# Kernel optimization log

Hardware: AMD Instinct MI355X
Metric: run time of the kernel (lower is better)

## Reference

```python
import jax, jax.numpy as jnp
import numpy as np

BS, DEG, H = 32, 4, 32
OUT = H  # n_aggr=1 inside Full -> out_size = n_aggr * h_size = h_size


def setup_inputs() -> dict:
    key = jax.random.key(0)
    k1, k2 = jax.random.split(key)
    neighbour_h = jax.random.normal(k1, (BS, DEG, H), dtype=jnp.float32)
    hp1 = H + 1
    t_shape = (hp1,) * DEG + (OUT,)  # [33,33,33,33,32]
    # xavier_uniform-like scale: fan_in = hp1**DEG, fan_out = OUT
    scale = float(np.sqrt(2.0 / (hp1 ** DEG + OUT)))
    T = jax.random.normal(k2, t_shape, dtype=jnp.float32) * scale
    return {"neighbour_h": neighbour_h, "T": T}


def reference(neighbour_h, T):
    # Full.forward: chunk neighbour_h along child dim, feed to AugmentedTensor.
    # AugmentedTensor: sequentially contract T against each child's augmented
    # embedding [h_i ; 1] over the leading axes of T.
    bs, deg, h = neighbour_h.shape
    hp1 = h + 1
    # augment with trailing 1 (bias slot): [bs, deg, h+1]
    h_aug = jnp.concatenate(
        [neighbour_h, jnp.ones((bs, deg, 1), neighbour_h.dtype)], axis=2
    )
    # first contraction: [bs, hp1] @ [hp1, hp1^(deg-1)*out]
    res = jnp.matmul(h_aug[:, 0, :], T.reshape(hp1, -1))
    # remaining contractions shrink the trailing dim by hp1 each step
    for i in range(1, deg):
        res = jnp.einsum("bi,bio->bo", h_aug[:, i, :], res.reshape(bs, hp1, -1))
    return res  # [bs, out_size] == [bs, h_size] since n_aggr=1
```

## Files before the change

kernel.cpp:

```cpp
#include <hip/hip_runtime.h>
#include <hip/hip_bf16.h>

#define HSZ 32
#define HP1 33
#define M3 35937
#define M3P 35952
#define TI_STRIDE 1149984
#define NBLK 2247
#define NT 64

#define OFF_A0T   0
#define OFF_D     8192
#define OFF_TILES 4610048

typedef short bf16x8 __attribute__((ext_vector_type(8)));
typedef float f32x16 __attribute__((ext_vector_type(16)));

__device__ inline short f2bf(float f) {
  __hip_bfloat16 h = __float2bfloat16(f);
  return __builtin_bit_cast(short, h);
}

__global__ __launch_bounds__(256) void k_pre(const float* __restrict__ nh,
                                             float* __restrict__ a0T,
                                             float* __restrict__ D,
                                             float* __restrict__ tiles) {
  const int b = blockIdx.y;
  const int m = blockIdx.x * 256 + threadIdx.x;
  if (m < M3P) {
    float v = 0.f;
    if (m < M3) {
      const int j = m / 1089;
      const int r = m - j * 1089;
      const int k = r / 33;
      const int l = r - k * 33;
      const float a1 = (j < HSZ) ? nh[(b * 4 + 1) * HSZ + j] : 1.0f;
      const float a2 = (k < HSZ) ? nh[(b * 4 + 2) * HSZ + k] : 1.0f;
      const float a3 = (l < HSZ) ? nh[(b * 4 + 3) * HSZ + l] : 1.0f;
      v = a1 * a2 * a3;
    }
    D[(size_t)b * M3P + m] = v;
  }
  if (blockIdx.x == 0 && threadIdx.x < HP1) {
    const int i = threadIdx.x;
    a0T[i * 32 + b] = (i < HSZ) ? nh[(b * 4 + 0) * HSZ + i] : 1.0f;
  }
  if (b == 1 && blockIdx.x < 64) {
    ((float4*)tiles)[blockIdx.x * 256 + threadIdx.x] =
        make_float4(0.f, 0.f, 0.f, 0.f);
  }
}

__global__ __launch_bounds__(64) void k_main(const float* __restrict__ T,
                                             const float* __restrict__ a0T,
                                             const float* __restrict__ D,
                                             float* __restrict__ tiles) {
  const int blk = blockIdx.x;
  const int m0 = blk * 16;
  const int l = (int)threadIdx.x;
  const int bo = l & 31;
  const int g = l >> 5;

  const float* dp = D + (size_t)bo * M3P + m0 + 8 * g;
  float df[8];
  *(float4*)(df)     = *(const float4*)(dp);
  *(float4*)(df + 4) = *(const float4*)(dp + 4);

  size_t toff[8];
#pragma unroll
  for (int e = 0; e < 8; ++e) {
    int mm = m0 + 8 * g + e;
    if (mm > M3 - 1) mm = M3 - 1;
    toff[e] = (size_t)mm * 32 + bo;
  }

  f32x16 acc = {};

  float tv[8];
#pragma unroll
  for (int e = 0; e < 8; ++e) tv[e] = T[toff[e]];
  float a0c = a0T[bo];

  for (int i = 0; i < HP1; ++i) {
    float tn[8];
    float a0n = 0.f;
    if (i < HP1 - 1) {
      const float* Tn = T + (size_t)(i + 1) * TI_STRIDE;
#pragma unroll
      for (int e = 0; e < 8; ++e) tn[e] = Tn[toff[e]];
      a0n = a0T[(i + 1) * 32 + bo];
    }
    bf16x8 af, bfr;
#pragma unroll
    for (int e = 0; e < 8; ++e) {
      af[e]  = f2bf(a0c * df[e]);
      bfr[e] = f2bf(tv[e]);
    }
    acc = __builtin_amdgcn_mfma_f32_32x32x16_bf16(af, bfr, acc, 0, 0, 0);
#pragma unroll
    for (int e = 0; e < 8; ++e) tv[e] = tn[e];
    a0c = a0n;
  }

  float* tp = tiles + (size_t)(blk & (NT - 1)) * 1024;
#pragma unroll
  for (int r = 0; r < 16; ++r) {
    const int brow = (r & 3) + 8 * (r >> 2) + 4 * g;
    atomicAdd(tp + brow * 32 + bo, acc[r]);
  }
}

__global__ __launch_bounds__(256) void k_red(const float* __restrict__ tiles,
                                             float* __restrict__ out) {
  const int idx = blockIdx.x * 256 + (int)threadIdx.x;
  float s = 0.f;
  for (int t = 0; t < NT; ++t) s += tiles[(size_t)t * 1024 + idx];
  out[idx] = s;
}

extern "C" void kernel_launch(void* const* d_in, const int* in_sizes, int n_in,
                              void* d_out, int out_size, void* d_ws, size_t ws_size,
                              hipStream_t stream) {
  const float* nh = (const float*)d_in[0];
  const float* T  = (const float*)d_in[1];
  float* out = (float*)d_out;
  char* ws = (char*)d_ws;
  float* a0T   = (float*)(ws + OFF_A0T);
  float* D     = (float*)(ws + OFF_D);
  float* tiles = (float*)(ws + OFF_TILES);

  k_pre<<<dim3(141, 32), 256, 0, stream>>>(nh, a0T, D, tiles);
  k_main<<<NBLK, 64, 0, stream>>>(T, a0T, D, tiles);
  k_red<<<4, 256, 0, stream>>>(tiles, out);
}
```

Baseline: 42.63 us.

## Stream T rows into LDS with async global_load_lds eight-deep pipeline

Result: faster. 40.18 us (-5.8%).

```diff
diff --git a/kernel.cpp b/kernel.cpp
--- a/kernel.cpp
+++ b/kernel.cpp
@@ -6,8 +6,10 @@
 #define M3 35937
 #define M3P 35952
 #define TI_STRIDE 1149984
+#define TIB ((size_t)TI_STRIDE * 4)
 #define NBLK 2247
 #define NT 64
+#define DEPTH 8
 
 #define OFF_A0T   0
 #define OFF_D     8192
@@ -55,6 +57,7 @@
                                              const float* __restrict__ a0T,
                                              const float* __restrict__ D,
                                              float* __restrict__ tiles) {
+  __shared__ float lds[DEPTH * 512];
   const int blk = blockIdx.x;
   const int m0 = blk * 16;
   const int l = (int)threadIdx.x;
@@ -66,41 +69,74 @@
   *(float4*)(df)     = *(const float4*)(dp);
   *(float4*)(df + 4) = *(const float4*)(dp + 4);
 
-  size_t toff[8];
+  float a0v[HP1];
 #pragma unroll
-  for (int e = 0; e < 8; ++e) {
-    int mm = m0 + 8 * g + e;
-    if (mm > M3 - 1) mm = M3 - 1;
-    toff[e] = (size_t)mm * 32 + bo;
+  for (int i = 0; i < HP1; ++i) a0v[i] = a0T[i * 32 + bo];
+
+  {
+    float dsum = 0.f, asum = 0.f;
+#pragma unroll
+    for (int e = 0; e < 8; ++e) dsum += df[e];
+#pragma unroll
+    for (int i = 0; i < HP1; ++i) asum += a0v[i];
+    asm volatile("" :: "v"(dsum), "v"(asum) : "memory");
   }
+
+  const int mrel = l >> 3;
+  const size_t src0 = (m0 + mrel < M3) ? ((size_t)(m0 * 32 + l * 4) * 4) : 0;
+  const size_t src1 =
+      (m0 + 8 + mrel < M3) ? ((size_t)(m0 * 32 + 256 + l * 4) * 4) : 0;
+  const char* Tb = (const char*)T;
+
+#define ISSUE(row_, slot_)                                                   \
+  {                                                                          \
+    const char* s0p_ = Tb + (size_t)(row_)*TIB + src0;                       \
+    const char* s1p_ = Tb + (size_t)(row_)*TIB + src1;                       \
+    __builtin_amdgcn_global_load_lds(                                        \
+        (const __attribute__((address_space(1))) void*)s0p_,                 \
+        (__attribute__((address_space(3))) void*)(&lds[(slot_)*512]),        \
+        16, 0, 0);                                                           \
+    __builtin_amdgcn_global_load_lds(                                        \
+        (const __attribute__((address_space(1))) void*)s1p_,                 \
+        (__attribute__((address_space(3))) void*)(&lds[(slot_)*512 + 256]),  \
+        16, 0, 0);                                                           \
+  }
+
+  ISSUE(0, 0) ISSUE(1, 1) ISSUE(2, 2) ISSUE(3, 3)
+  ISSUE(4, 4) ISSUE(5, 5) ISSUE(6, 6) ISSUE(7, 7)
 
   f32x16 acc = {};
 
-  float tv[8];
-#pragma unroll
-  for (int e = 0; e < 8; ++e) tv[e] = T[toff[e]];
-  float a0c = a0T[bo];
+#define STEP(i_, vm_, doIssue_)                                              \
+  {                                                                          \
+    asm volatile("s_waitcnt vmcnt(" #vm_ ")" ::: "memory");                  \
+    __builtin_amdgcn_sched_barrier(0);                                       \
+    float tvv[8];                                                            \
+    _Pragma("unroll")                                                        \
+    for (int e = 0; e < 8; ++e)                                              \
+      tvv[e] = lds[((i_) % DEPTH) * 512 + (8 * g + e) * 32 + bo];            \
+    asm volatile("s_waitcnt lgkmcnt(0)" ::: "memory");                       \
+    if (doIssue_) ISSUE((i_) + DEPTH, (i_) % DEPTH)                          \
+    bf16x8 af, bfr;                                                          \
+    _Pragma("unroll")                                                        \
+    for (int e = 0; e < 8; ++e) {                                            \
+      af[e] = f2bf(a0v[i_] * df[e]);                                         \
+      bfr[e] = f2bf(tvv[e]);                                                 \
+    }                                                                        \
+    acc = __builtin_amdgcn_mfma_f32_32x32x16_bf16(af, bfr, acc, 0, 0, 0);    \
+  }
 
-  for (int i = 0; i < HP1; ++i) {
-    float tn[8];
-    float a0n = 0.f;
-    if (i < HP1 - 1) {
-      const float* Tn = T + (size_t)(i + 1) * TI_STRIDE;
-#pragma unroll
-      for (int e = 0; e < 8; ++e) tn[e] = Tn[toff[e]];
-      a0n = a0T[(i + 1) * 32 + bo];
-    }
-    bf16x8 af, bfr;
-#pragma unroll
-    for (int e = 0; e < 8; ++e) {
-      af[e]  = f2bf(a0c * df[e]);
-      bfr[e] = f2bf(tv[e]);
-    }
-    acc = __builtin_amdgcn_mfma_f32_32x32x16_bf16(af, bfr, acc, 0, 0, 0);
-#pragma unroll
-    for (int e = 0; e < 8; ++e) tv[e] = tn[e];
-    a0c = a0n;
-  }
+  STEP(0, 14, 1)  STEP(1, 14, 1)  STEP(2, 14, 1)  STEP(3, 14, 1)
+  STEP(4, 14, 1)  STEP(5, 14, 1)  STEP(6, 14, 1)  STEP(7, 14, 1)
+  STEP(8, 14, 1)  STEP(9, 14, 1)  STEP(10, 14, 1) STEP(11, 14, 1)
+  STEP(12, 14, 1) STEP(13, 14, 1) STEP(14, 14, 1) STEP(15, 14, 1)
+  STEP(16, 14, 1) STEP(17, 14, 1) STEP(18, 14, 1) STEP(19, 14, 1)
+  STEP(20, 14, 1) STEP(21, 14, 1) STEP(22, 14, 1) STEP(23, 14, 1)
+  STEP(24, 14, 1) STEP(25, 14, 0) STEP(26, 12, 0) STEP(27, 10, 0)
+  STEP(28, 8, 0)  STEP(29, 6, 0)  STEP(30, 4, 0)  STEP(31, 2, 0)
+  STEP(32, 0, 0)
+#undef STEP
+#undef ISSUE
 
   float* tp = tiles + (size_t)(blk & (NT - 1)) * 1024;
 #pragma unroll
```

## Stream T through LDS with async global_load_lds multi-stage pipeline, double work per block

Applied to the files above, without the earlier changes.

After: 39.75 us. 1.07x faster.

```diff
diff --git a/kernel.cpp b/kernel.cpp
--- a/kernel.cpp
+++ b/kernel.cpp
@@ -4,14 +4,16 @@
 #define HSZ 32
 #define HP1 33
 #define M3 35937
-#define M3P 35952
+#define M3P2 35968
 #define TI_STRIDE 1149984
-#define NBLK 2247
+#define TIB ((size_t)TI_STRIDE * 4)
+#define NBLK 1124
 #define NT 64
+#define DEPTH 6
 
 #define OFF_A0T   0
 #define OFF_D     8192
-#define OFF_TILES 4610048
+#define OFF_TILES 4612096
 
 typedef short bf16x8 __attribute__((ext_vector_type(8)));
 typedef float f32x16 __attribute__((ext_vector_type(16)));
@@ -27,7 +29,7 @@
                                              float* __restrict__ tiles) {
   const int b = blockIdx.y;
   const int m = blockIdx.x * 256 + threadIdx.x;
-  if (m < M3P) {
+  if (m < M3P2) {
     float v = 0.f;
     if (m < M3) {
       const int j = m / 1089;
@@ -39,7 +41,7 @@
       const float a3 = (l < HSZ) ? nh[(b * 4 + 3) * HSZ + l] : 1.0f;
       v = a1 * a2 * a3;
     }
-    D[(size_t)b * M3P + m] = v;
+    D[(size_t)b * M3P2 + m] = v;
   }
   if (blockIdx.x == 0 && threadIdx.x < HP1) {
     const int i = threadIdx.x;
@@ -55,52 +57,94 @@
                                              const float* __restrict__ a0T,
                                              const float* __restrict__ D,
                                              float* __restrict__ tiles) {
+  __shared__ float lds[DEPTH * 1024];
   const int blk = blockIdx.x;
-  const int m0 = blk * 16;
+  const int m0 = blk * 32;
   const int l = (int)threadIdx.x;
   const int bo = l & 31;
   const int g = l >> 5;
 
-  const float* dp = D + (size_t)bo * M3P + m0 + 8 * g;
-  float df[8];
-  *(float4*)(df)     = *(const float4*)(dp);
-  *(float4*)(df + 4) = *(const float4*)(dp + 4);
+  const float* dp = D + (size_t)bo * M3P2 + m0 + 8 * g;
+  float df0[8], df1[8];
+  *(float4*)(df0)     = *(const float4*)(dp);
+  *(float4*)(df0 + 4) = *(const float4*)(dp + 4);
+  *(float4*)(df1)     = *(const float4*)(dp + 16);
+  *(float4*)(df1 + 4) = *(const float4*)(dp + 20);
 
-  size_t toff[8];
+  float a0v[HP1];
 #pragma unroll
-  for (int e = 0; e < 8; ++e) {
-    int mm = m0 + 8 * g + e;
-    if (mm > M3 - 1) mm = M3 - 1;
-    toff[e] = (size_t)mm * 32 + bo;
+  for (int i = 0; i < HP1; ++i) a0v[i] = a0T[i * 32 + bo];
+
+  {
+    float s = 0.f;
+#pragma unroll
+    for (int e = 0; e < 8; ++e) s += df0[e] + df1[e];
+#pragma unroll
+    for (int i = 0; i < HP1; ++i) s += a0v[i];
+    asm volatile("" :: "v"(s) : "memory");
   }
+
+  const int mrel = l >> 3;
+  size_t src[4];
+#pragma unroll
+  for (int q = 0; q < 4; ++q) {
+    const bool valid = (m0 + 8 * q + mrel) < M3;
+    src[q] = valid ? ((size_t)(m0 * 32 + q * 256 + l * 4) * 4) : 0;
+  }
+  const char* Tb = (const char*)T;
+
+#define ISSUE(row_, slot_)                                                    \
+  {                                                                           \
+    _Pragma("unroll")                                                         \
+    for (int q = 0; q < 4; ++q) {                                             \
+      __builtin_amdgcn_global_load_lds(                                       \
+          (const __attribute__((address_space(1))) void*)(                    \
+              Tb + (size_t)(row_)*TIB + src[q]),                              \
+          (__attribute__((address_space(3))) void*)(                          \
+              &lds[(slot_)*1024 + q * 256]),                                  \
+          16, 0, 0);                                                          \
+    }                                                                         \
+  }
+
+  ISSUE(0, 0) ISSUE(1, 1) ISSUE(2, 2) ISSUE(3, 3) ISSUE(4, 4) ISSUE(5, 5)
 
   f32x16 acc = {};
 
-  float tv[8];
-#pragma unroll
-  for (int e = 0; e < 8; ++e) tv[e] = T[toff[e]];
-  float a0c = a0T[bo];
+#define STEP(i_, vm_, doIssue_)                                               \
+  {                                                                           \
+    asm volatile("s_waitcnt vmcnt(" #vm_ ")" ::: "memory");                   \
+    __builtin_amdgcn_sched_barrier(0);                                        \
+    float tv0[8], tv1[8];                                                     \
+    _Pragma("unroll")                                                         \
+    for (int e = 0; e < 8; ++e) {                                             \
+      tv0[e] = lds[((i_) % DEPTH) * 1024 + (8 * g + e) * 32 + bo];            \
+      tv1[e] = lds[((i_) % DEPTH) * 1024 + 512 + (8 * g + e) * 32 + bo];      \
+    }                                                                         \
+    asm volatile("s_waitcnt lgkmcnt(0)" ::: "memory");                        \
+    if (doIssue_) ISSUE((i_) + DEPTH, (i_) % DEPTH)                           \
+    bf16x8 af0, bf0, af1, bf1;                                                \
+    _Pragma("unroll")                                                         \
+    for (int e = 0; e < 8; ++e) {                                             \
+      af0[e] = f2bf(a0v[i_] * df0[e]);                                        \
+      bf0[e] = f2bf(tv0[e]);                                                  \
+      af1[e] = f2bf(a0v[i_] * df1[e]);                                        \
+      bf1[e] = f2bf(tv1[e]);                                                  \
+    }                                                                         \
+    acc = __builtin_amdgcn_mfma_f32_32x32x16_bf16(af0, bf0, acc, 0, 0, 0);    \
+    acc = __builtin_amdgcn_mfma_f32_32x32x16_bf16(af1, bf1, acc, 0, 0, 0);    \
+  }
 
-  for (int i = 0; i < HP1; ++i) {
-    float tn[8];
-    float a0n = 0.f;
-    if (i < HP1 - 1) {
-      const float* Tn = T + (size_t)(i + 1) * TI_STRIDE;
-#pragma unroll
-      for (int e = 0; e < 8; ++e) tn[e] = Tn[toff[e]];
-      a0n = a0T[(i + 1) * 32 + bo];
-    }
-    bf16x8 af, bfr;
-#pragma unroll
-    for (int e = 0; e < 8; ++e) {
-      af[e]  = f2bf(a0c * df[e]);
-      bfr[e] = f2bf(tv[e]);
-    }
-    acc = __builtin_amdgcn_mfma_f32_32x32x16_bf16(af, bfr, acc, 0, 0, 0);
-#pragma unroll
-    for (int e = 0; e < 8; ++e) tv[e] = tn[e];
-    a0c = a0n;
-  }
+  STEP(0, 20, 1)  STEP(1, 20, 1)  STEP(2, 20, 1)  STEP(3, 20, 1)
+  STEP(4, 20, 1)  STEP(5, 20, 1)  STEP(6, 20, 1)  STEP(7, 20, 1)
+  STEP(8, 20, 1)  STEP(9, 20, 1)  STEP(10, 20, 1) STEP(11, 20, 1)
+  STEP(12, 20, 1) STEP(13, 20, 1) STEP(14, 20, 1) STEP(15, 20, 1)
+  STEP(16, 20, 1) STEP(17, 20, 1) STEP(18, 20, 1) STEP(19, 20, 1)
+  STEP(20, 20, 1) STEP(21, 20, 1) STEP(22, 20, 1) STEP(23, 20, 1)
+  STEP(24, 20, 1) STEP(25, 20, 1) STEP(26, 20, 1) STEP(27, 20, 0)
+  STEP(28, 16, 0) STEP(29, 12, 0) STEP(30, 8, 0)  STEP(31, 4, 0)
+  STEP(32, 0, 0)
+#undef STEP
+#undef ISSUE
 
   float* tp = tiles + (size_t)(blk & (NT - 1)) * 1024;
 #pragma unroll
```
